# Kernel tuning notes

Measured on AMD Instinct MI355X. Metric: run time of the kernel, lower is better.

The kernel has to match this reference:

```python
import jax, jax.numpy as jnp
import numpy as np

N, D, E, NNZ = 200000, 128, 1024, 1600000


def setup_inputs() -> dict:
    key = jax.random.key(0)
    ks = jax.random.split(key, 8)
    x = jax.random.normal(ks[0], (N, D), jnp.float32)
    tb_W = jax.random.normal(ks[1], (5, 3, D, D), jnp.float32) * 0.05
    tb_b = jax.random.normal(ks[2], (5, 3, D), jnp.float32) * 0.05
    hg_W = jax.random.normal(ks[3], (2, D, D), jnp.float32) * 0.05
    hg_b = jax.random.normal(ks[4], (2, D), jnp.float32) * 0.05
    hyperedge_attr = jax.random.normal(ks[5], (E, D), jnp.float32)
    node_idx = jax.random.randint(ks[6], (NNZ,), 0, N)
    edge_idx = jax.random.randint(ks[7], (NNZ,), 0, E)
    return dict(x=x, tb_W=tb_W, tb_b=tb_b, hg_W=hg_W, hg_b=hg_b,
                hyperedge_attr=hyperedge_attr, node_idx=node_idx,
                edge_idx=edge_idx, num_hyperedges=E)


def _time_block(x, W, b):
    # 1x1 Conv2d over channel dim == per-node linear. W:[3,D,D], b:[3,D]
    c1 = x @ W[0] + b[0]
    c2 = x @ W[1] + b[1]
    c3 = x @ W[2] + b[2]
    return jax.nn.relu(c1 + jax.nn.sigmoid(c2) + c3)


def _hypergraph_conv(x, node_idx, edge_idx, W, b, num_nodes, num_edges):
    # PyG HypergraphConv, use_attention=False (heads=1):
    # out = D^{-1} H B H^T (x W) + b, H given as COO (node_idx, edge_idx)
    xp = x @ W
    ones = jnp.ones(node_idx.shape[0], xp.dtype)
    Dn = jax.ops.segment_sum(ones, node_idx, num_segments=num_nodes)
    Dn = jnp.where(Dn > 0, 1.0 / Dn, 0.0)
    Be = jax.ops.segment_sum(ones, edge_idx, num_segments=num_edges)
    Be = jnp.where(Be > 0, 1.0 / Be, 0.0)
    # node -> hyperedge aggregation, normalized by 1/B_e
    m = jax.ops.segment_sum(xp[node_idx], edge_idx, num_segments=num_edges) * Be[:, None]
    # hyperedge -> node aggregation, normalized by 1/D_v
    out = jax.ops.segment_sum(m[edge_idx], node_idx, num_segments=num_nodes) * Dn[:, None]
    return out + b


def reference(x, tb_W, tb_b, hg_W, hg_b, hyperedge_attr, node_idx, edge_idx, num_hyperedges):
    # hyperedge_attr is unused when use_attention=False (faithful to PyG)
    n = x.shape[0]
    h = _time_block(x, tb_W[0], tb_b[0])
    h = _hypergraph_conv(h, node_idx, edge_idx, hg_W[0], hg_b[0], n, num_hyperedges)
    h = _time_block(h, tb_W[1], tb_b[1])
    h = _time_block(h, tb_W[2], tb_b[2])
    h = _hypergraph_conv(h, node_idx, edge_idx, hg_W[1], hg_b[1], n, num_hyperedges)
    h = _time_block(h, tb_W[3], tb_b[3])
    h = _time_block(h, tb_W[4], tb_b[4])
    return h
```

## Files before the change

kernel.cpp:

```cpp
#include <hip/hip_runtime.h>
#include <stdint.h>

#define N_NODES 200000
#define DIM     128
#define N_EDGES 1024
#define NNZ_C   1600000
#define NT_TILES 6250

#define NBLK   250
#define CHUNK  6400
#define ITERS  25
#define NCB    196

#define NG_BLOCKS 2048
#define NG_WAVES  (NG_BLOCKS*4)

typedef __attribute__((ext_vector_type(8))) short short8;
typedef __attribute__((ext_vector_type(4))) float f32x4;

__device__ __forceinline__ float u2f(uint32_t u){ union{uint32_t u;float f;} x; x.u=u; return x.f; }
__device__ __forceinline__ uint32_t f2u(float f){ union{uint32_t u;float f;} x; x.f=f; return x.u; }
__device__ __forceinline__ unsigned short f2bf(float f){
  uint32_t u = f2u(f);
  u += 0x7fffu + ((u >> 16) & 1u);
  return (unsigned short)(u >> 16);
}

__global__ void prep_tb_w(const float* __restrict__ W, short* __restrict__ Wt){
  int i = blockIdx.x*256 + threadIdx.x;
  if (i >= 5*384*128) return;
  int k   = i & 127;
  int col = (i >> 7) % 384;
  int s   = i / 49152;
  int j = col >> 7, n = col & 127;
  Wt[i] = (short)f2bf(W[((s*3 + j)*128 + k)*128 + n]);
}
__global__ void prep_hg_wf(const float* __restrict__ W, float* __restrict__ Wtf){
  int i = blockIdx.x*256 + threadIdx.x;
  if (i >= 2*128*128) return;
  int k = i & 127;
  int n = (i >> 7) & 127;
  int g = i >> 14;
  Wtf[i] = W[(g*128 + k)*128 + n];
}

__global__ __launch_bounds__(256) void hist_kernel(
    const int* __restrict__ nidx, const int* __restrict__ eidx,
    int* __restrict__ ebh, int* __restrict__ nbh)
{
  __shared__ int eh[N_EDGES];
  __shared__ int nh[NCB];
  int tid = threadIdx.x, blk = blockIdx.x;
  #pragma unroll
  for (int l = tid; l < N_EDGES; l += 256) eh[l] = 0;
  for (int l = tid; l < NCB; l += 256) nh[l] = 0;
  __syncthreads();
  int base = blk*CHUNK;
  for (int it = 0; it < ITERS; it++){
    int i = base + it*256 + tid;
    atomicAdd(&eh[eidx[i]], 1);
    atomicAdd(&nh[nidx[i] >> 10], 1);
  }
  __syncthreads();
  for (int l = tid; l < N_EDGES; l += 256) ebh[blk*N_EDGES + l] = eh[l];
  for (int l = tid; l < NCB; l += 256) nbh[blk*NCB + l] = nh[l];
}

__global__ __launch_bounds__(1024) void escan_kernel(
    int* __restrict__ ebh, int* __restrict__ eoff)
{
  __shared__ int sc[1024];
  int e = threadIdx.x;
  int total = 0;
  #pragma unroll 10
  for (int b = 0; b < NBLK; b++){
    int idx = b*N_EDGES + e;
    int t = ebh[idx];
    ebh[idx] = total;
    total += t;
  }
  sc[e] = total; __syncthreads();
  for (int off=1; off<1024; off<<=1){
    int v = (e >= off) ? sc[e-off] : 0;
    __syncthreads();
    sc[e] += v;
    __syncthreads();
  }
  int base = sc[e] - total;
  eoff[e] = base;
  if (e == 1023) eoff[1024] = sc[1023];
  #pragma unroll 10
  for (int b = 0; b < NBLK; b++) ebh[b*N_EDGES + e] += base;
}

__global__ __launch_bounds__(256) void nscan_kernel(
    int* __restrict__ nbh, int* __restrict__ cbase)
{
  __shared__ int sc[256];
  int c = threadIdx.x;
  int total = 0;
  if (c < NCB){
    #pragma unroll 10
    for (int b = 0; b < NBLK; b++){
      int idx = b*NCB + c;
      int t = nbh[idx];
      nbh[idx] = total;
      total += t;
    }
  }
  sc[c] = (c < NCB) ? total : 0; __syncthreads();
  for (int off=1; off<256; off<<=1){
    int v = (c >= off) ? sc[c-off] : 0;
    __syncthreads();
    sc[c] += v;
    __syncthreads();
  }
  int base = sc[c] - ((c < NCB) ? total : 0);
  if (c < NCB) cbase[c] = base;
  if (c == NCB-1) cbase[NCB] = sc[c];
  __syncthreads();
  if (c < NCB){
    #pragma unroll 10
    for (int b = 0; b < NBLK; b++) nbh[b*NCB + c] += base;
  }
}

__global__ __launch_bounds__(256) void scatter_kernel(
    const int* __restrict__ nidx, const int* __restrict__ eidx,
    const int* __restrict__ ebh, const int* __restrict__ nbh,
    int* __restrict__ enodes, uint32_t* __restrict__ pairs)
{
  __shared__ int cure[N_EDGES];
  __shared__ int curn[NCB];
  int tid = threadIdx.x, blk = blockIdx.x;
  for (int l = tid; l < N_EDGES; l += 256) cure[l] = ebh[blk*N_EDGES + l];
  for (int l = tid; l < NCB; l += 256)     curn[l] = nbh[blk*NCB + l];
  __syncthreads();
  int base = blk*CHUNK;
  for (int it = 0; it < ITERS; it++){
    int i = base + it*256 + tid;
    int v = nidx[i], e = eidx[i];
    int pe = atomicAdd(&cure[e], 1);
    enodes[pe] = v;
    int pn = atomicAdd(&curn[v >> 10], 1);
    pairs[pn] = ((uint32_t)v << 10) | (uint32_t)e;
  }
}

__global__ __launch_bounds__(256) void node_build_kernel(
    const uint32_t* __restrict__ pairs, const int* __restrict__ cbase,
    int* __restrict__ noff, int* __restrict__ nedges)
{
  __shared__ int cnt[1024];
  __shared__ int off[1024];
  __shared__ int part[256];
  int tid = threadIdx.x, c = blockIdx.x;
  int n0 = c << 10;
  int nloc = min(1024, N_NODES - n0);
  int s = cbase[c], e = cbase[c+1];
  #pragma unroll
  for (int l = tid; l < 1024; l += 256) cnt[l] = 0;
  __syncthreads();
  for (int i = s + tid; i < e; i += 256)
    atomicAdd(&cnt[(pairs[i] >> 10) & 1023], 1);
  __syncthreads();
  int c0 = cnt[tid*4], c1 = cnt[tid*4+1], c2 = cnt[tid*4+2], c3 = cnt[tid*4+3];
  int sum = c0+c1+c2+c3;
  part[tid] = sum; __syncthreads();
  for (int o=1; o<256; o<<=1){
    int v = (tid >= o) ? part[tid-o] : 0;
    __syncthreads();
    part[tid] += v;
    __syncthreads();
  }
  int pb = part[tid] - sum;
  off[tid*4]   = pb;
  off[tid*4+1] = pb + c0;
  off[tid*4+2] = pb + c0 + c1;
  off[tid*4+3] = pb + c0 + c1 + c2;
  __syncthreads();
  for (int l = tid; l < nloc; l += 256) noff[n0 + l] = s + off[l];
  if (c == 0 && tid == 0) noff[N_NODES] = NNZ_C;
  __syncthreads();
  for (int i = s + tid; i < e; i += 256){
    uint32_t p = pairs[i];
    int local = (p >> 10) & 1023;
    int pos = s + atomicAdd(&off[local], 1);
    nedges[pos] = (int)(p & 1023);
  }
}

template<bool IN_F32, int OUT_MODE>
__global__ __launch_bounds__(256, 2) void gemm_kernel(
    const void* __restrict__ in, void* __restrict__ out,
    const short* __restrict__ Wt, const float* __restrict__ bias)
{
  __shared__ short Atile[32][136];
  const int tid  = threadIdx.x;
  const int lane = tid & 63;
  const int w    = tid >> 6;
  const int l15  = lane & 15;
  const int quad = lane >> 4;

  short8 bfrag[3][2][4];
  #pragma unroll
  for (int j = 0; j < 3; j++)
    #pragma unroll
    for (int nt = 0; nt < 2; nt++){
      const short* bp = Wt + (j*128 + w*32 + nt*16 + l15)*128 + quad*8;
      #pragma unroll
      for (int ks = 0; ks < 4; ks++)
        bfrag[j][nt][ks] = *(const short8*)(bp + ks*32);
    }

  float bv[3][2];
  #pragma unroll
  for (int j = 0; j < 3; j++)
    #pragma unroll
    for (int nt = 0; nt < 2; nt++)
      bv[j][nt] = bias[j*128 + w*32 + nt*16 + l15];

  const int arow = tid >> 3;
  const int aseg = (tid & 7) * 2;

  short8 pre0, pre1;
  auto loadA = [&](int t){
    int off = (t*32 + arow)*128 + aseg*8;
    if (IN_F32){
      const float* f = (const float*)in + off;
      f32x4 q0 = ((const f32x4*)f)[0];
      f32x4 q1 = ((const f32x4*)f)[1];
      f32x4 q2 = ((const f32x4*)f)[2];
      f32x4 q3 = ((const f32x4*)f)[3];
      short8 t0, t1;
      #pragma unroll
      for (int u = 0; u < 4; u++){
        t0[u]   = (short)f2bf(q0[u]);
        t0[u+4] = (short)f2bf(q1[u]);
        t1[u]   = (short)f2bf(q2[u]);
        t1[u+4] = (short)f2bf(q3[u]);
      }
      pre0 = t0; pre1 = t1;
    } else {
      const short* hp = (const short*)in + off;
      pre0 = *(const short8*)hp;
      pre1 = *(const short8*)(hp + 8);
    }
  };

  int t = blockIdx.x;
  loadA(t);
  for (;;){
    __syncthreads();
    *(short8*)&Atile[arow][aseg*8]     = pre0;
    *(short8*)&Atile[arow][aseg*8 + 8] = pre1;
    __syncthreads();
    int tn = t + gridDim.x;
    if (tn < NT_TILES) loadA(tn);

    const int base = t*32;
    #pragma unroll
    for (int rt = 0; rt < 2; rt++){
      short8 af[4];
      #pragma unroll
      for (int ks = 0; ks < 4; ks++)
        af[ks] = *(const short8*)&Atile[rt*16 + l15][ks*32 + quad*8];

      f32x4 acc[3][2];
      #pragma unroll
      for (int j = 0; j < 3; j++)
        #pragma unroll
        for (int nt = 0; nt < 2; nt++){
          acc[j][nt] = (f32x4){0.f, 0.f, 0.f, 0.f};
          #pragma unroll
          for (int ks = 0; ks < 4; ks++)
            acc[j][nt] = __builtin_amdgcn_mfma_f32_16x16x32_bf16(
                af[ks], bfrag[j][nt][ks], acc[j][nt], 0, 0, 0);
        }

      #pragma unroll
      for (int nt = 0; nt < 2; nt++){
        int col = w*32 + nt*16 + l15;
        #pragma unroll
        for (int r = 0; r < 4; r++){
          int row = base + rt*16 + quad*4 + r;
          float c2 = acc[1][nt][r] + bv[1][nt];
          float sg = 1.f / (1.f + __expf(-c2));
          float v = acc[0][nt][r] + bv[0][nt] + sg + acc[2][nt][r] + bv[2][nt];
          v = fmaxf(v, 0.f);
          if (OUT_MODE == 1) ((float*)out)[row*128 + col] = v;
          else if (OUT_MODE == 0) ((unsigned short*)out)[row*128 + col] = f2bf(v);
          else {
            int pk = __builtin_amdgcn_cvt_pk_fp8_f32(v, v, 0, false);
            ((unsigned char*)out)[row*128 + col] = (unsigned char)(pk & 0xff);
          }
        }
      }
    }
    if (tn >= NT_TILES) break;
    t = tn;
  }
}

__device__ __forceinline__ void acc16(float* a, uint4 r){
  uint32_t w[4] = {r.x, r.y, r.z, r.w};
  #pragma unroll
  for (int q = 0; q < 4; q++){
    auto lo = __builtin_amdgcn_cvt_pk_f32_fp8(w[q], false);
    auto hi = __builtin_amdgcn_cvt_pk_f32_fp8(w[q], true);
    a[q*4+0] += lo[0]; a[q*4+1] += lo[1]; a[q*4+2] += hi[0]; a[q*4+3] += hi[1];
  }
}

__global__ __launch_bounds__(256) void edge_gather_kernel(
    const unsigned char* __restrict__ h8, const int* __restrict__ eoff,
    const int* __restrict__ enodes, float* __restrict__ s_e)
{
  int e = blockIdx.x;
  int s = eoff[e], en = eoff[e+1];
  int tid  = threadIdx.x;
  int slot = tid >> 3;
  int ch   = tid & 7;
  const size_t choff = (size_t)ch * 16;

  float a[16];
  #pragma unroll
  for (int j = 0; j < 16; j++) a[j] = 0.f;

  int i0 = s + slot;
  int n0 = (i0      < en) ? enodes[i0]      : -1;
  int n1 = (i0 + 32 < en) ? enodes[i0 + 32] : -1;
  int n2 = (i0 + 64 < en) ? enodes[i0 + 64] : -1;
  int n3 = (i0 + 96 < en) ? enodes[i0 + 96] : -1;

  while (i0 < en){
    int i1 = i0 + 128;
    int m0 = (i1      < en) ? enodes[i1]      : -1;
    int m1 = (i1 + 32 < en) ? enodes[i1 + 32] : -1;
    int m2 = (i1 + 64 < en) ? enodes[i1 + 64] : -1;
    int m3 = (i1 + 96 < en) ? enodes[i1 + 96] : -1;

    uint4 r0 = *(const uint4*)(h8 + (((size_t)max(n0,0)) << 7) + choff);
    uint4 r1 = *(const uint4*)(h8 + (((size_t)max(n1,0)) << 7) + choff);
    uint4 r2 = *(const uint4*)(h8 + (((size_t)max(n2,0)) << 7) + choff);
    uint4 r3 = *(const uint4*)(h8 + (((size_t)max(n3,0)) << 7) + choff);
    if (n0 < 0) r0 = make_uint4(0,0,0,0);
    if (n1 < 0) r1 = make_uint4(0,0,0,0);
    if (n2 < 0) r2 = make_uint4(0,0,0,0);
    if (n3 < 0) r3 = make_uint4(0,0,0,0);

    acc16(a, r0); acc16(a, r1); acc16(a, r2); acc16(a, r3);

    n0 = m0; n1 = m1; n2 = m2; n3 = m3;
    i0 = i1;
  }

  __shared__ float red[32][132];
  #pragma unroll
  for (int j = 0; j < 16; j++) red[slot][ch*16 + j] = a[j];
  __syncthreads();
  if (tid < 128){
    float sum = 0.f;
    #pragma unroll
    for (int r = 0; r < 32; r++) sum += red[r][tid];
    s_e[e*128 + tid] = sum;
  }
}

__global__ __launch_bounds__(128) void egemm_kernel(
    const float* __restrict__ s_e, const int* __restrict__ eoff,
    const float* __restrict__ Wtf, uint32_t* __restrict__ mbf)
{
  __shared__ float srow[128];
  __shared__ float sacc[128];
  int e = blockIdx.x, n = threadIdx.x;
  srow[n] = s_e[e*128 + n];
  __syncthreads();
  int deg = eoff[e+1] - eoff[e];
  float be = deg > 0 ? 1.f/(float)deg : 0.f;
  const f32x4* w4 = (const f32x4*)(Wtf + n*128);
  float acc = 0.f;
  #pragma unroll
  for (int k = 0; k < 32; k++){
    f32x4 qv = w4[k];
    acc += qv[0]*srow[k*4] + qv[1]*srow[k*4+1] + qv[2]*srow[k*4+2] + qv[3]*srow[k*4+3];
  }
  sacc[n] = acc * be;
  __syncthreads();
  if (n < 64){
    uint32_t lo = f2bf(sacc[2*n]);
    uint32_t hi = f2bf(sacc[2*n+1]);
    mbf[e*64 + n] = (hi << 16) | lo;
  }
}

__global__ __launch_bounds__(256) void node_gather_kernel(
    const uint32_t* __restrict__ mbf, const int* __restrict__ noff,
    const int* __restrict__ nedges, const float* __restrict__ hb,
    uint32_t* __restrict__ outp)
{
  int wid  = (blockIdx.x << 2) | (threadIdx.x >> 6);
  int lane = threadIdx.x & 63;
  float b0 = hb[2*lane], b1 = hb[2*lane+1];
  const int K = (N_NODES + NG_WAVES - 1) / NG_WAVES;
  int v0 = wid * K;
  int v1 = min(v0 + K, N_NODES);
  for (int v = v0; v < v1; v++){
    int s = noff[v], e = noff[v+1];
    float a0 = 0.f, a1 = 0.f, a2 = 0.f, a3 = 0.f;
    int i = s;
    for (; i + 4 <= e; i += 4){
      int e0 = nedges[i],   e1 = nedges[i+1];
      int e2 = nedges[i+2], e3 = nedges[i+3];
      uint32_t r0 = mbf[(e0 << 6) | lane];
      uint32_t r1 = mbf[(e1 << 6) | lane];
      uint32_t r2 = mbf[(e2 << 6) | lane];
      uint32_t r3 = mbf[(e3 << 6) | lane];
      a0 += u2f(r0 << 16); a1 += u2f(r0 & 0xffff0000u);
      a2 += u2f(r1 << 16); a3 += u2f(r1 & 0xffff0000u);
      a0 += u2f(r2 << 16); a1 += u2f(r2 & 0xffff0000u);
      a2 += u2f(r3 << 16); a3 += u2f(r3 & 0xffff0000u);
    }
    for (; i < e; i++){
      int ed = nedges[i];
      uint32_t r = mbf[(ed << 6) | lane];
      a0 += u2f(r << 16); a1 += u2f(r & 0xffff0000u);
    }
    a0 += a2; a1 += a3;
    float dn = (e > s) ? 1.f/(float)(e - s) : 0.f;
    uint32_t lo = f2bf(a0*dn + b0);
    uint32_t hi = f2bf(a1*dn + b1);
    outp[((size_t)v << 6) | lane] = (hi << 16) | lo;
  }
}

extern "C" void kernel_launch(void* const* d_in, const int* in_sizes, int n_in,
                              void* d_out, int out_size, void* d_ws, size_t ws_size,
                              hipStream_t stream)
{
  (void)in_sizes; (void)n_in; (void)out_size; (void)ws_size;
  const float* x   = (const float*)d_in[0];
  const float* tbW = (const float*)d_in[1];
  const float* tbb = (const float*)d_in[2];
  const float* hgW = (const float*)d_in[3];
  const float* hgb = (const float*)d_in[4];
  const int* nidx  = (const int*)d_in[6];
  const int* eidx  = (const int*)d_in[7];
  float* out = (float*)d_out;

  char* p = (char*)d_ws;
  auto alloc = [&](size_t sz){ void* r = (void*)p; p += (sz + 255) & ~(size_t)255; return r; };
  unsigned short* hA = (unsigned short*)alloc((size_t)N_NODES*DIM*2);
  unsigned short* hB = (unsigned short*)alloc((size_t)N_NODES*DIM*2);
  unsigned char*  h8 = (unsigned char*)alloc((size_t)N_NODES*DIM);
  float* s_e  = (float*)alloc((size_t)N_EDGES*DIM*4);
  uint32_t* mbf = (uint32_t*)alloc((size_t)N_EDGES*64*4);
  short* WtTb = (short*)alloc((size_t)5*384*128*2);
  float* Wtf  = (float*)alloc((size_t)2*128*128*4);
  int* ebh  = (int*)alloc((size_t)NBLK*N_EDGES*4);
  int* nbh  = (int*)alloc((size_t)NBLK*NCB*4);
  int* eoff = (int*)alloc((N_EDGES+1)*4);
  int* cbase= (int*)alloc((NCB+1)*4);
  int* noff = (int*)alloc((size_t)(N_NODES+1)*4);
  int* enodes = (int*)alloc((size_t)NNZ_C*4);
  int* nedges = (int*)alloc((size_t)NNZ_C*4);
  uint32_t* pairs = (uint32_t*)h8;

  prep_tb_w<<<960, 256, 0, stream>>>(tbW, WtTb);
  prep_hg_wf<<<128, 256, 0, stream>>>(hgW, Wtf);

  hist_kernel<<<NBLK, 256, 0, stream>>>(nidx, eidx, ebh, nbh);
  escan_kernel<<<1, 1024, 0, stream>>>(ebh, eoff);
  nscan_kernel<<<1, 256, 0, stream>>>(nbh, cbase);
  scatter_kernel<<<NBLK, 256, 0, stream>>>(nidx, eidx, ebh, nbh, enodes, pairs);
  node_build_kernel<<<NCB, 256, 0, stream>>>(pairs, cbase, noff, nedges);

  gemm_kernel<true, 2><<<1024, 256, 0, stream>>>(x, h8, WtTb, tbb);
  edge_gather_kernel<<<N_EDGES, 256, 0, stream>>>(h8, eoff, enodes, s_e);
  egemm_kernel<<<N_EDGES, 128, 0, stream>>>(s_e, eoff, Wtf, mbf);
  node_gather_kernel<<<NG_BLOCKS, 256, 0, stream>>>(mbf, noff, nedges, hgb, (uint32_t*)hA);
  gemm_kernel<false, 0><<<1024, 256, 0, stream>>>(hA, hB, WtTb + 1*49152, tbb + 1*384);
  gemm_kernel<false, 2><<<1024, 256, 0, stream>>>(hB, h8, WtTb + 2*49152, tbb + 2*384);
  edge_gather_kernel<<<N_EDGES, 256, 0, stream>>>(h8, eoff, enodes, s_e);
  egemm_kernel<<<N_EDGES, 128, 0, stream>>>(s_e, eoff, Wtf + 16384, mbf);
  node_gather_kernel<<<NG_BLOCKS, 256, 0, stream>>>(mbf, noff, nedges, hgb + 128, (uint32_t*)hA);
  gemm_kernel<false, 0><<<1024, 256, 0, stream>>>(hA, hB, WtTb + 3*49152, tbb + 3*384);
  gemm_kernel<false, 1><<<1024, 256, 0, stream>>>(hB, out, WtTb + 4*49152, tbb + 4*384);
}
```

Before: 681.4 us.

## Stage per-wave node edge lists in LDS and unroll node gather by eight

The node gather kernel now has each wave load the edge-index range for its 25 nodes into shared memory with coalesced reads. It then issues eight independent mbf row loads per iteration, clamping past-the-end slots to the last valid edge and subtracting the duplicated contributions afterwards. Edge indices are pre-shifted to byte offsets at build time, and the node end offsets are held in lanes and fetched with readlane, which removes per-node scalar loads and address arithmetic. This is meant to cut index-load latency and raise memory-level parallelism. In exchange it adds a block barrier, LDS use, a fallback path for waves whose range exceeds the stage size, and extra work on padded iterations.

```diff
diff --git a/kernel.cpp b/kernel.cpp
--- a/kernel.cpp
+++ b/kernel.cpp
@@ -12,8 +12,10 @@
 #define ITERS  25
 #define NCB    196
 
-#define NG_BLOCKS 2048
+#define NG_BLOCKS 2000
 #define NG_WAVES  (NG_BLOCKS*4)
+#define NG_K      25
+#define NG_STAGE  512
 
 typedef __attribute__((ext_vector_type(8))) short short8;
 typedef __attribute__((ext_vector_type(4))) float f32x4;
@@ -186,7 +188,7 @@
     uint32_t p = pairs[i];
     int local = (p >> 10) & 1023;
     int pos = s + atomicAdd(&off[local], 1);
-    nedges[pos] = (int)(p & 1023);
+    nedges[pos] = (int)((p & 1023) << 8);
   }
 }
 
@@ -399,38 +401,74 @@
     const int* __restrict__ nedges, const float* __restrict__ hb,
     uint32_t* __restrict__ outp)
 {
-  int wid  = (blockIdx.x << 2) | (threadIdx.x >> 6);
-  int lane = threadIdx.x & 63;
-  float b0 = hb[2*lane], b1 = hb[2*lane+1];
-  const int K = (N_NODES + NG_WAVES - 1) / NG_WAVES;
-  int v0 = wid * K;
-  int v1 = min(v0 + K, N_NODES);
-  for (int v = v0; v < v1; v++){
-    int s = noff[v], e = noff[v+1];
-    float a0 = 0.f, a1 = 0.f, a2 = 0.f, a3 = 0.f;
-    int i = s;
-    for (; i + 4 <= e; i += 4){
-      int e0 = nedges[i],   e1 = nedges[i+1];
-      int e2 = nedges[i+2], e3 = nedges[i+3];
-      uint32_t r0 = mbf[(e0 << 6) | lane];
-      uint32_t r1 = mbf[(e1 << 6) | lane];
-      uint32_t r2 = mbf[(e2 << 6) | lane];
-      uint32_t r3 = mbf[(e3 << 6) | lane];
-      a0 += u2f(r0 << 16); a1 += u2f(r0 & 0xffff0000u);
-      a2 += u2f(r1 << 16); a3 += u2f(r1 & 0xffff0000u);
-      a0 += u2f(r2 << 16); a1 += u2f(r2 & 0xffff0000u);
-      a2 += u2f(r3 << 16); a3 += u2f(r3 & 0xffff0000u);
+  __shared__ int sidx[4][NG_STAGE];
+  const int wslot = threadIdx.x >> 6;
+  const int wid   = (blockIdx.x << 2) | wslot;
+  const int lane  = threadIdx.x & 63;
+  const int lane4 = lane << 2;
+  const float b0 = hb[2*lane], b1 = hb[2*lane+1];
+  const int v0 = wid * NG_K;
+
+  int eArr = noff[min(v0 + 1 + lane, N_NODES)];
+  int sW   = __builtin_amdgcn_readfirstlane(noff[v0]);
+  int send = __builtin_amdgcn_readlane(eArr, NG_K - 1);
+  int n = send - sW;
+
+  int* myIdx = sidx[wslot];
+  bool useLds = (n <= NG_STAGE);
+  if (useLds){
+    for (int b = lane; b < n; b += 64) myIdx[b] = nedges[sW + b];
+  }
+  __syncthreads();
+
+  const char* mb = (const char*)mbf;
+  if (useLds){
+    int s = sW;
+    for (int vr = 0; vr < NG_K; vr++){
+      int e = __builtin_amdgcn_readlane(eArr, vr);
+      float a0 = 0.f, a1 = 0.f;
+      uint32_t rlast = 0;
+      for (int i = s; i < e; i += 8){
+        uint32_t r[8];
+        #pragma unroll
+        for (int k = 0; k < 8; k++){
+          int li = min(i + k, e - 1) - sW;
+          r[k] = *(const uint32_t*)(mb + (myIdx[li] + lane4));
+        }
+        #pragma unroll
+        for (int k = 0; k < 8; k++){
+          a0 += u2f(r[k] << 16);
+          a1 += u2f(r[k] & 0xffff0000u);
+        }
+        rlast = r[7];
+      }
+      int d = e - s;
+      float dead = (float)(((d + 7) & ~7) - d);
+      a0 -= dead * u2f(rlast << 16);
+      a1 -= dead * u2f(rlast & 0xffff0000u);
+      float dn = (d > 0) ? 1.f/(float)d : 0.f;
+      uint32_t lo = f2bf(a0*dn + b0);
+      uint32_t hi = f2bf(a1*dn + b1);
+      outp[((size_t)(v0 + vr) << 6) | lane] = (hi << 16) | lo;
+      s = e;
     }
-    for (; i < e; i++){
-      int ed = nedges[i];
-      uint32_t r = mbf[(ed << 6) | lane];
-      a0 += u2f(r << 16); a1 += u2f(r & 0xffff0000u);
+  } else {
+    int s = sW;
+    for (int vr = 0; vr < NG_K; vr++){
+      int e = __builtin_amdgcn_readlane(eArr, vr);
+      float a0 = 0.f, a1 = 0.f;
+      for (int i = s; i < e; i++){
+        uint32_t r = *(const uint32_t*)(mb + (nedges[i] + lane4));
+        a0 += u2f(r << 16);
+        a1 += u2f(r & 0xffff0000u);
+      }
+      int d = e - s;
+      float dn = (d > 0) ? 1.f/(float)d : 0.f;
+      uint32_t lo = f2bf(a0*dn + b0);
+      uint32_t hi = f2bf(a1*dn + b1);
+      outp[((size_t)(v0 + vr) << 6) | lane] = (hi << 16) | lo;
+      s = e;
     }
-    a0 += a2; a1 += a3;
-    float dn = (e > s) ? 1.f/(float)(e - s) : 0.f;
-    uint32_t lo = f2bf(a0*dn + b0);
-    uint32_t hi = f2bf(a1*dn + b1);
-    outp[((size_t)v << 6) | lane] = (hi << 16) | lo;
   }
 }
 
@@ -463,7 +501,7 @@
   int* cbase= (int*)alloc((NCB+1)*4);
   int* noff = (int*)alloc((size_t)(N_NODES+1)*4);
   int* enodes = (int*)alloc((size_t)NNZ_C*4);
-  int* nedges = (int*)alloc((size_t)NNZ_C*4);
+  int* nedges = (int*)alloc((size_t)NNZ_C*4 + 64);
   uint32_t* pairs = (uint32_t*)h8;
 
   prep_tb_w<<<960, 256, 0, stream>>>(tbW, WtTb);
```

Result: faster. 655.5 us (-3.8%).
